# Optimization experiments

Measured on AMD Instinct MI355X. Metric: run time of the kernel, lower is better.

Reference implementation:

```python
import jax, jax.numpy as jnp
import numpy as np

N_NODES = 20000
N_EDGES = 640000
D = 64        # node / edge feature dim
H = 128       # MLP hidden dim


def setup_inputs() -> dict:
    key = jax.random.key(0)
    ks = jax.random.split(key, 12)
    inp = {
        "x": jax.random.normal(ks[0], (N_NODES, D), dtype=jnp.float32),
        "edge_index": jax.random.randint(ks[1], (2, N_EDGES), 0, N_NODES, dtype=jnp.int64),
        "edge_attr": jax.random.normal(ks[2], (N_EDGES, D), dtype=jnp.float32),
        "f": jax.random.normal(ks[3], (N_NODES, D), dtype=jnp.float32),
        # edge MLP: concat(x_src, x_dest, edge_attr) = 3D -> H -> D
        "We1": jax.random.normal(ks[4], (3 * D, H), dtype=jnp.float32) / np.sqrt(3 * D),
        "be1": jnp.zeros((H,), dtype=jnp.float32),
        "We2": jax.random.normal(ks[5], (H, D), dtype=jnp.float32) / np.sqrt(H),
        "be2": jnp.zeros((D,), dtype=jnp.float32),
        # node MLP: concat(x, agg, f) = 3D -> H -> D
        "Wn1": jax.random.normal(ks[6], (3 * D, H), dtype=jnp.float32) / np.sqrt(3 * D),
        "bn1": jnp.zeros((H,), dtype=jnp.float32),
        "Wn2": jax.random.normal(ks[7], (H, D), dtype=jnp.float32) / np.sqrt(H),
        "bn2": jnp.zeros((D,), dtype=jnp.float32),
    }
    return inp


def reference(x, edge_index, edge_attr, f, We1, be1, We2, be2, Wn1, bn1, Wn2, bn2):
    src, dest = edge_index[0], edge_index[1]
    # edge model: MLP over gathered src/dest node features + edge attrs
    e_in = jnp.concatenate([x[src], x[dest], edge_attr], axis=-1)      # [E, 3D]
    e_h = jax.nn.relu(e_in @ We1 + be1)                                 # [E, H]
    edge_out = e_h @ We2 + be2                                          # [E, D]
    # node model: scatter-add edge messages to dest, then MLP
    agg = jax.ops.segment_sum(edge_out, dest, num_segments=N_NODES)    # [N, D]
    n_in = jnp.concatenate([x, agg, f], axis=-1)                        # [N, 3D]
    n_h = jax.nn.relu(n_in @ Wn1 + bn1)                                 # [N, H]
    x_out = n_h @ Wn2 + bn2                                             # [N, D]
    return (x_out, edge_out)
```

## Files before the change

### kernel.cpp

```cpp
#include <hip/hip_runtime.h>

#define NE 640000
#define NN 20000
#define SEI 200
#define SEH 136
#define SEO 100

typedef __attribute__((ext_vector_type(8))) short s16x8;
typedef __attribute__((ext_vector_type(4))) short s16x4;
typedef __attribute__((ext_vector_type(4))) float f32x4;

typedef const __attribute__((ext_vector_type(4))) float cf32x4;

#define BARRIER_LGKM() do {                                   \
    asm volatile("s_waitcnt lgkmcnt(0)" ::: "memory");        \
    __builtin_amdgcn_s_barrier();                             \
    __builtin_amdgcn_sched_barrier(0);                        \
  } while (0)

__device__ __forceinline__ short f2bf(float f) {
  unsigned int u = __float_as_uint(f);
  u += 0x7fffu + ((u >> 16) & 1u);
  return (short)(u >> 16);
}

__device__ __forceinline__ s16x8 cvt8(f32x4 a, f32x4 b) {
  s16x8 o;
  o[0]=f2bf(a[0]); o[1]=f2bf(a[1]); o[2]=f2bf(a[2]); o[3]=f2bf(a[3]);
  o[4]=f2bf(b[0]); o[5]=f2bf(b[1]); o[6]=f2bf(b[2]); o[7]=f2bf(b[3]);
  return o;
}

__device__ __forceinline__ void load_wfrags_lds(const float* W1, const float* W2,
                                                const float* b1, const float* b2,
                                                short* smem, int t,
                                                int wv, int r, int g,
                                                s16x8 w1f[2][6], s16x8 w2f[4],
                                                f32x4 b1r[2], f32x4* b2r) {
  #pragma unroll
  for (int i = 0; i < 24; ++i) {
    int idx4 = t + i * 256;
    f32x4 v = ((cf32x4*)W1)[idx4];
    s16x4 pk; pk[0]=f2bf(v[0]); pk[1]=f2bf(v[1]); pk[2]=f2bf(v[2]); pk[3]=f2bf(v[3]);
    *(s16x4*)&smem[idx4 * 4] = pk;
  }
  __syncthreads();
  #pragma unroll
  for (int nn = 0; nn < 2; ++nn) {
    const int h = (wv*2+nn)*16 + r;
    #pragma unroll
    for (int kk = 0; kk < 6; ++kk) {
      s16x8 wf;
      #pragma unroll
      for (int i = 0; i < 8; ++i) wf[i] = smem[(kk*32 + g*8 + i)*128 + h];
      w1f[nn][kk] = wf;
    }
    b1r[nn] = *(cf32x4*)(b1 + (wv*2+nn)*16 + g*4);
  }
  __syncthreads();
  #pragma unroll
  for (int i = 0; i < 8; ++i) {
    int idx4 = t + i * 256;
    f32x4 v = ((cf32x4*)W2)[idx4];
    s16x4 pk; pk[0]=f2bf(v[0]); pk[1]=f2bf(v[1]); pk[2]=f2bf(v[2]); pk[3]=f2bf(v[3]);
    *(s16x4*)&smem[idx4 * 4] = pk;
  }
  __syncthreads();
  {
    const int h2 = wv*16 + r;
    #pragma unroll
    for (int kk = 0; kk < 4; ++kk) {
      s16x8 wf;
      #pragma unroll
      for (int i = 0; i < 8; ++i) wf[i] = smem[(kk*32 + g*8 + i)*64 + h2];
      w2f[kk] = wf;
    }
    *b2r = *(cf32x4*)(b2 + wv*16 + g*4);
  }
  __syncthreads();
}


__global__ void count_kernel(const int* __restrict__ eidx, int* __restrict__ cursor) {
  const int4* d4 = (const int4*)(eidx + NE);
  int i = blockIdx.x * blockDim.x + threadIdx.x;
  if (i < NE / 4) {
    int4 d = d4[i];
    atomicAdd(&cursor[d.x], 1);
    atomicAdd(&cursor[d.y], 1);
    atomicAdd(&cursor[d.z], 1);
    atomicAdd(&cursor[d.w], 1);
  }
}

__global__ __launch_bounds__(1024)
void scan_kernel(int* __restrict__ cursor, int* __restrict__ offs) {
  __shared__ int cnt[20480];
  __shared__ int part[1024];
  const int t = threadIdx.x;
  for (int i = t; i < 20480; i += 1024)
    cnt[i] = (i < NN) ? cursor[i] : 0;
  __syncthreads();
  const int lo = t * 20;
  int s = 0;
  #pragma unroll
  for (int k = 0; k < 20; ++k) s += cnt[lo + k];
  part[t] = s;
  __syncthreads();
  for (int d = 1; d < 1024; d <<= 1) {
    int u = (t >= d) ? part[t - d] : 0;
    __syncthreads();
    part[t] += u;
    __syncthreads();
  }
  int run = part[t] - s;
  #pragma unroll
  for (int k = 0; k < 20; ++k) {
    int c = cnt[lo + k];
    cnt[lo + k] = run;
    run += c;
  }
  __syncthreads();
  for (int i = t; i < NN; i += 1024) {
    int v = cnt[i];
    offs[i] = v;
    cursor[i] = v;
  }
  if (t == 1023) offs[NN] = NE;
}

__global__ void scatter_kernel(const int* __restrict__ eidx,
                               int* __restrict__ cursor, int* __restrict__ elist) {
  const int4* d4 = (const int4*)(eidx + NE);
  int i = blockIdx.x * blockDim.x + threadIdx.x;
  if (i < NE / 4) {
    int4 d = d4[i];
    const int e = i * 4;
    elist[atomicAdd(&cursor[d.x], 1)] = e;
    elist[atomicAdd(&cursor[d.y], 1)] = e + 1;
    elist[atomicAdd(&cursor[d.z], 1)] = e + 2;
    elist[atomicAdd(&cursor[d.w], 1)] = e + 3;
  }
}

#define LOAD_ROWS(sv, dv, ee) do {                                        \
    cf32x4* ps_ = (cf32x4*)(x  + (size_t)(sv)*64 + p*16);                 \
    cf32x4* pd_ = (cf32x4*)(x  + (size_t)(dv)*64 + p*16);                 \
    cf32x4* pe_ = (cf32x4*)(ea + (size_t)(ee)*64 + p*16);                 \
    L[0]=ps_[0]; L[1]=ps_[1]; L[2]=ps_[2];  L[3]=ps_[3];                  \
    L[4]=pd_[0]; L[5]=pd_[1]; L[6]=pd_[2];  L[7]=pd_[3];                  \
    L[8]=pe_[0]; L[9]=pe_[1]; L[10]=pe_[2]; L[11]=pe_[3];                 \
  } while (0)

#define WRITE_EIN(buf) do {                                               \
    short* stg_ = (buf) + el*SEI + p*16;                                  \
    ((s16x8*)stg_)[0]       = cvt8(L[0], L[1]);                           \
    ((s16x8*)stg_)[1]       = cvt8(L[2], L[3]);                           \
    ((s16x8*)(stg_+64))[0]  = cvt8(L[4], L[5]);                           \
    ((s16x8*)(stg_+64))[1]  = cvt8(L[6], L[7]);                           \
    ((s16x8*)(stg_+128))[0] = cvt8(L[8], L[9]);                           \
    ((s16x8*)(stg_+128))[1] = cvt8(L[10], L[11]);                         \
  } while (0)

__global__ __launch_bounds__(256, 2)
void edge_kernel(const float* __restrict__ x, const int* __restrict__ eidx,
                 const float* __restrict__ ea, const int* __restrict__ elist,
                 const float* __restrict__ We1, const float* __restrict__ be1,
                 const float* __restrict__ We2, const float* __restrict__ be2,
                 float* __restrict__ edge_out, float* __restrict__ agg)
{
  __shared__ __align__(16) char smem[69632];
  short* sEin0 = (short*)smem;
  short* sEin1 = (short*)(smem + 25600);
  short* sEh   = (short*)(smem + 51200);
  int* sDest0  = (int*)(smem + 68608);
  int* sDest1  = (int*)(smem + 68864);
  int* sEid0   = (int*)(smem + 69120);
  int* sEid1   = (int*)(smem + 69376);

  const int t = threadIdx.x;
  const int wv = t >> 6, lane = t & 63;
  const int r = lane & 15, g = lane >> 4;

  s16x8 w1f[2][6], w2f[4];
  f32x4 b1r[2], b2r;
  load_wfrags_lds(We1, We2, be1, be2, (short*)smem, t, wv, r, g,
                  w1f, w2f, b1r, &b2r);

  const int el = t >> 2, p = t & 3;
  const f32x4 zero = {0.f, 0.f, 0.f, 0.f};

  const int b = blockIdx.x;
  const int t0 = b * 19 + (b < 272 ? b : 272);
  const int t1 = t0 + (b < 272 ? 20 : 19);

  f32x4 L[12];
  int eW = 0, dW = 0;
  int eI = 0, sI = 0, dI = 0;
  int tile = t0;

  {
    int e0 = elist[(tile << 6) + el];
    int s0 = eidx[e0], d0 = eidx[NE + e0];
    LOAD_ROWS(s0, d0, e0);
    WRITE_EIN(sEin0);
    if (p == 0) { sDest0[el] = d0; sEid0[el] = e0; }
    if (tile + 1 < t1) {
      eW = elist[((tile + 1) << 6) + el];
      int sv = eidx[eW]; dW = eidx[NE + eW];
      LOAD_ROWS(sv, dW, eW);
    }
    if (tile + 2 < t1) {
      eI = elist[((tile + 2) << 6) + el];
      sI = eidx[eI]; dI = eidx[NE + eI];
    }
  }
  BARRIER_LGKM();

  int cur = 0;
  while (tile < t1) {
    const short* Ecur = cur ? sEin1 : sEin0;
    short* Enxt = cur ? sEin0 : sEin1;
    float* EoutC = (float*)(cur ? (smem + 25600) : smem);
    const int* sDestC = cur ? sDest1 : sDest0;
    const int* sEidC  = cur ? sEid1  : sEid0;
    int* sDestN = cur ? sDest0 : sDest1;
    int* sEidN  = cur ? sEid0  : sEid1;

    const int tW = tile + 1, tI = tile + 2, tX = tile + 3;
    if (tW < t1) {
      WRITE_EIN(Enxt);
      if (p == 0) { sDestN[el] = dW; sEidN[el] = eW; }
    }
    if (tI < t1) { LOAD_ROWS(sI, dI, eI); eW = eI; dW = dI; }
    if (tX < t1) {
      eI = elist[(tX << 6) + el];
      sI = eidx[eI]; dI = eidx[NE + eI];
    }

    f32x4 acc1[2][4];
    #pragma unroll
    for (int nn = 0; nn < 2; ++nn)
      #pragma unroll
      for (int j = 0; j < 4; ++j) acc1[nn][j] = zero;
    #pragma unroll
    for (int kk = 0; kk < 6; ++kk) {
      #pragma unroll
      for (int j = 0; j < 4; ++j) {
        s16x8 ef = *(const s16x8*)&Ecur[(j*16 + r)*SEI + kk*32 + g*8];
        acc1[0][j] = __builtin_amdgcn_mfma_f32_16x16x32_bf16(w1f[0][kk], ef, acc1[0][j], 0, 0, 0);
        acc1[1][j] = __builtin_amdgcn_mfma_f32_16x16x32_bf16(w1f[1][kk], ef, acc1[1][j], 0, 0, 0);
      }
    }
    #pragma unroll
    for (int nn = 0; nn < 2; ++nn)
      #pragma unroll
      for (int j = 0; j < 4; ++j) {
        s16x4 pk;
        #pragma unroll
        for (int q = 0; q < 4; ++q) {
          float v = acc1[nn][j][q] + b1r[nn][q];
          pk[q] = f2bf(v > 0.f ? v : 0.f);
        }
        *(s16x4*)&sEh[(j*16 + r)*SEH + (wv*2+nn)*16 + g*4] = pk;
      }
    BARRIER_LGKM();

    #pragma unroll
    for (int j = 0; j < 4; ++j) {
      f32x4 a2 = zero;
      #pragma unroll
      for (int kk = 0; kk < 4; ++kk) {
        s16x8 hf = *(const s16x8*)&sEh[(j*16 + r)*SEH + kk*32 + g*8];
        a2 = __builtin_amdgcn_mfma_f32_16x16x32_bf16(w2f[kk], hf, a2, 0, 0, 0);
      }
      a2 += b2r;
      const int eg = sEidC[j*16 + r];
      *(f32x4*)&edge_out[(size_t)eg*64 + wv*16 + g*4] = a2;
      *(f32x4*)&EoutC[(j*16 + r)*SEO + wv*16 + g*4] = a2;
    }
    BARRIER_LGKM();

    {
      const int row0 = wv * 16;
      float acc = EoutC[row0*SEO + lane];
      int dcur = sDestC[row0];
      #pragma unroll
      for (int k = 1; k < 16; ++k) {
        const int dn = sDestC[row0 + k];
        const float v = EoutC[(row0 + k)*SEO + lane];
        if (dn != dcur) {
          unsafeAtomicAdd(&agg[(size_t)dcur*64 + lane], acc);
          acc = v; dcur = dn;
        } else {
          acc += v;
        }
      }
      unsafeAtomicAdd(&agg[(size_t)dcur*64 + lane], acc);
    }
    cur ^= 1;
    tile = tW;
  }
}

__global__ __launch_bounds__(256, 2)
void node_kernel(const float* __restrict__ x, const float* agg,
                 const float* __restrict__ f,
                 const float* __restrict__ Wn1, const float* __restrict__ bn1,
                 const float* __restrict__ Wn2, const float* __restrict__ bn2,
                 float* x_out)
{
  __shared__ __align__(16) char smem[49152];
  short* sEin = (short*)smem;
  short* sEh  = (short*)(smem + 25600);

  const int t = threadIdx.x;
  const int wv = t >> 6, lane = t & 63;
  const int r = lane & 15, g = lane >> 4;

  s16x8 w1f[2][6], w2f[4];
  f32x4 b1r[2], b2r;
  load_wfrags_lds(Wn1, Wn2, bn1, bn2, (short*)smem, t, wv, r, g,
                  w1f, w2f, b1r, &b2r);

  const int el = t >> 2, p = t & 3;
  const f32x4 zero = {0.f, 0.f, 0.f, 0.f};
  const int nT = (NN + 63) / 64;

  for (int tile = blockIdx.x; tile < nT; tile += (int)gridDim.x) {
    const int base = tile << 6;
    const int i = base + el;

    f32x4 L[12];
    if (i < NN) {
      cf32x4* ps_ = (cf32x4*)(x   + (size_t)i*64 + p*16);
      cf32x4* pa_ = (cf32x4*)(agg + (size_t)i*64 + p*16);
      cf32x4* pf_ = (cf32x4*)(f   + (size_t)i*64 + p*16);
      L[0]=ps_[0]; L[1]=ps_[1]; L[2]=ps_[2];  L[3]=ps_[3];
      L[4]=pa_[0]; L[5]=pa_[1]; L[6]=pa_[2];  L[7]=pa_[3];
      L[8]=pf_[0]; L[9]=pf_[1]; L[10]=pf_[2]; L[11]=pf_[3];
    } else {
      #pragma unroll
      for (int q = 0; q < 12; ++q) L[q] = zero;
    }
    WRITE_EIN(sEin);
    __syncthreads();

    f32x4 acc1[2][4];
    #pragma unroll
    for (int nn = 0; nn < 2; ++nn)
      #pragma unroll
      for (int j = 0; j < 4; ++j) acc1[nn][j] = zero;
    #pragma unroll
    for (int kk = 0; kk < 6; ++kk) {
      #pragma unroll
      for (int j = 0; j < 4; ++j) {
        s16x8 ef = *(const s16x8*)&sEin[(j*16 + r)*SEI + kk*32 + g*8];
        acc1[0][j] = __builtin_amdgcn_mfma_f32_16x16x32_bf16(w1f[0][kk], ef, acc1[0][j], 0, 0, 0);
        acc1[1][j] = __builtin_amdgcn_mfma_f32_16x16x32_bf16(w1f[1][kk], ef, acc1[1][j], 0, 0, 0);
      }
    }
    #pragma unroll
    for (int nn = 0; nn < 2; ++nn)
      #pragma unroll
      for (int j = 0; j < 4; ++j) {
        s16x4 pk;
        #pragma unroll
        for (int q = 0; q < 4; ++q) {
          float v = acc1[nn][j][q] + b1r[nn][q];
          pk[q] = f2bf(v > 0.f ? v : 0.f);
        }
        *(s16x4*)&sEh[(j*16 + r)*SEH + (wv*2+nn)*16 + g*4] = pk;
      }
    __syncthreads();

    #pragma unroll
    for (int j = 0; j < 4; ++j) {
      f32x4 a2 = zero;
      #pragma unroll
      for (int kk = 0; kk < 4; ++kk) {
        s16x8 hf = *(const s16x8*)&sEh[(j*16 + r)*SEH + kk*32 + g*8];
        a2 = __builtin_amdgcn_mfma_f32_16x16x32_bf16(w2f[kk], hf, a2, 0, 0, 0);
      }
      const int row = base + j*16 + r;
      if (row < NN) {
        f32x4 v = a2 + b2r;
        *(f32x4*)&x_out[(size_t)row*64 + wv*16 + g*4] = v;
      }
    }
  }
}

extern "C" void kernel_launch(void* const* d_in, const int* in_sizes, int n_in,
                              void* d_out, int out_size, void* d_ws, size_t ws_size,
                              hipStream_t stream) {
  const float* x   = (const float*)d_in[0];
  const int*   ei  = (const int*)d_in[1];
  const float* ea  = (const float*)d_in[2];
  const float* f   = (const float*)d_in[3];
  const float* We1 = (const float*)d_in[4];
  const float* be1 = (const float*)d_in[5];
  const float* We2 = (const float*)d_in[6];
  const float* be2 = (const float*)d_in[7];
  const float* Wn1 = (const float*)d_in[8];
  const float* bn1 = (const float*)d_in[9];
  const float* Wn2 = (const float*)d_in[10];
  const float* bn2 = (const float*)d_in[11];

  float* x_out    = (float*)d_out;
  float* edge_out = x_out + (size_t)NN * 64;

  int* cursor = (int*)d_ws;
  int* offs   = cursor + NN;
  int* elist  = offs + NN + 8;

  hipMemsetAsync(x_out, 0, (size_t)NN * 64 * sizeof(float), stream);
  hipMemsetAsync(cursor, 0, NN * sizeof(int), stream);
  count_kernel<<<625, 256, 0, stream>>>(ei, cursor);
  scan_kernel<<<1, 1024, 0, stream>>>(cursor, offs);
  scatter_kernel<<<625, 256, 0, stream>>>(ei, cursor, elist);
  edge_kernel<<<512, 256, 0, stream>>>(x, ei, ea, elist, We1, be1, We2, be2,
                                       edge_out, x_out);
  node_kernel<<<105, 256, 0, stream>>>(x, x_out, f, Wn1, bn1, Wn2, bn2, x_out);
}
```

Baseline: 227.4 us.

## Widen edge kernel to 512 threads, splitting MLP work across eight waves

The edge kernel moves from 256 to 512 threads per block. Each of the eight waves now owns one 16-column slice of the hidden layer and half of the output-row tiles, and each thread gathers half as many row bytes. This cuts per-thread registers (weight fragments, accumulators, load buffers) so more waves can hide the latency of the irregular gathers. The cost is more barrier participants per block and smaller per-wave segment reductions, which issue more atomics to agg.

```diff
diff --git a/kernel.cpp b/kernel.cpp
--- a/kernel.cpp
+++ b/kernel.cpp
@@ -35,8 +35,56 @@
                                                 const float* b1, const float* b2,
                                                 short* smem, int t,
                                                 int wv, int r, int g,
-                                                s16x8 w1f[2][6], s16x8 w2f[4],
-                                                f32x4 b1r[2], f32x4* b2r) {
+                                                s16x8 w1f[6], s16x8 w2f[4],
+                                                f32x4* b1r, f32x4* b2r) {
+  #pragma unroll
+  for (int i = 0; i < 12; ++i) {
+    int idx4 = t + i * 512;
+    f32x4 v = ((cf32x4*)W1)[idx4];
+    s16x4 pk; pk[0]=f2bf(v[0]); pk[1]=f2bf(v[1]); pk[2]=f2bf(v[2]); pk[3]=f2bf(v[3]);
+    *(s16x4*)&smem[idx4 * 4] = pk;
+  }
+  __syncthreads();
+  {
+    const int h = wv*16 + r;
+    #pragma unroll
+    for (int kk = 0; kk < 6; ++kk) {
+      s16x8 wf;
+      #pragma unroll
+      for (int i = 0; i < 8; ++i) wf[i] = smem[(kk*32 + g*8 + i)*128 + h];
+      w1f[kk] = wf;
+    }
+    *b1r = *(cf32x4*)(b1 + wv*16 + g*4);
+  }
+  __syncthreads();
+  #pragma unroll
+  for (int i = 0; i < 4; ++i) {
+    int idx4 = t + i * 512;
+    f32x4 v = ((cf32x4*)W2)[idx4];
+    s16x4 pk; pk[0]=f2bf(v[0]); pk[1]=f2bf(v[1]); pk[2]=f2bf(v[2]); pk[3]=f2bf(v[3]);
+    *(s16x4*)&smem[idx4 * 4] = pk;
+  }
+  __syncthreads();
+  {
+    const int h2 = (wv >> 1)*16 + r;
+    #pragma unroll
+    for (int kk = 0; kk < 4; ++kk) {
+      s16x8 wf;
+      #pragma unroll
+      for (int i = 0; i < 8; ++i) wf[i] = smem[(kk*32 + g*8 + i)*64 + h2];
+      w2f[kk] = wf;
+    }
+    *b2r = *(cf32x4*)(b2 + (wv >> 1)*16 + g*4);
+  }
+  __syncthreads();
+}
+
+__device__ __forceinline__ void load_wfrags_lds4(const float* W1, const float* W2,
+                                                 const float* b1, const float* b2,
+                                                 short* smem, int t,
+                                                 int wv, int r, int g,
+                                                 s16x8 w1f[2][6], s16x8 w2f[4],
+                                                 f32x4 b1r[2], f32x4* b2r) {
   #pragma unroll
   for (int i = 0; i < 24; ++i) {
     int idx4 = t + i * 256;
@@ -144,25 +192,22 @@
 }
 
 #define LOAD_ROWS(sv, dv, ee) do {                                        \
-    cf32x4* ps_ = (cf32x4*)(x  + (size_t)(sv)*64 + p*16);                 \
-    cf32x4* pd_ = (cf32x4*)(x  + (size_t)(dv)*64 + p*16);                 \
-    cf32x4* pe_ = (cf32x4*)(ea + (size_t)(ee)*64 + p*16);                 \
-    L[0]=ps_[0]; L[1]=ps_[1]; L[2]=ps_[2];  L[3]=ps_[3];                  \
-    L[4]=pd_[0]; L[5]=pd_[1]; L[6]=pd_[2];  L[7]=pd_[3];                  \
-    L[8]=pe_[0]; L[9]=pe_[1]; L[10]=pe_[2]; L[11]=pe_[3];                 \
+    cf32x4* ps_ = (cf32x4*)(x  + (size_t)(sv)*64 + p*8);                  \
+    cf32x4* pd_ = (cf32x4*)(x  + (size_t)(dv)*64 + p*8);                  \
+    cf32x4* pe_ = (cf32x4*)(ea + (size_t)(ee)*64 + p*8);                  \
+    L[0]=ps_[0]; L[1]=ps_[1];                                             \
+    L[2]=pd_[0]; L[3]=pd_[1];                                             \
+    L[4]=pe_[0]; L[5]=pe_[1];                                             \
   } while (0)
 
 #define WRITE_EIN(buf) do {                                               \
-    short* stg_ = (buf) + el*SEI + p*16;                                  \
-    ((s16x8*)stg_)[0]       = cvt8(L[0], L[1]);                           \
-    ((s16x8*)stg_)[1]       = cvt8(L[2], L[3]);                           \
-    ((s16x8*)(stg_+64))[0]  = cvt8(L[4], L[5]);                           \
-    ((s16x8*)(stg_+64))[1]  = cvt8(L[6], L[7]);                           \
-    ((s16x8*)(stg_+128))[0] = cvt8(L[8], L[9]);                           \
-    ((s16x8*)(stg_+128))[1] = cvt8(L[10], L[11]);                         \
+    short* stg_ = (buf) + el*SEI + p*8;                                   \
+    *(s16x8*)stg_         = cvt8(L[0], L[1]);                             \
+    *(s16x8*)(stg_ + 64)  = cvt8(L[2], L[3]);                             \
+    *(s16x8*)(stg_ + 128) = cvt8(L[4], L[5]);                             \
   } while (0)
 
-__global__ __launch_bounds__(256, 2)
+__global__ __launch_bounds__(512, 2)
 void edge_kernel(const float* __restrict__ x, const int* __restrict__ eidx,
                  const float* __restrict__ ea, const int* __restrict__ elist,
                  const float* __restrict__ We1, const float* __restrict__ be1,
@@ -182,19 +227,19 @@
   const int wv = t >> 6, lane = t & 63;
   const int r = lane & 15, g = lane >> 4;
 
-  s16x8 w1f[2][6], w2f[4];
-  f32x4 b1r[2], b2r;
+  s16x8 w1f[6], w2f[4];
+  f32x4 b1r, b2r;
   load_wfrags_lds(We1, We2, be1, be2, (short*)smem, t, wv, r, g,
-                  w1f, w2f, b1r, &b2r);
-
-  const int el = t >> 2, p = t & 3;
+                  w1f, w2f, &b1r, &b2r);
+
+  const int el = t >> 3, p = t & 7;
   const f32x4 zero = {0.f, 0.f, 0.f, 0.f};
 
   const int b = blockIdx.x;
   const int t0 = b * 19 + (b < 272 ? b : 272);
   const int t1 = t0 + (b < 272 ? 20 : 19);
 
-  f32x4 L[12];
+  f32x4 L[6];
   int eW = 0, dW = 0;
   int eI = 0, sI = 0, dI = 0;
   int tile = t0;
@@ -238,55 +283,54 @@
       sI = eidx[eI]; dI = eidx[NE + eI];
     }
 
-    f32x4 acc1[2][4];
-    #pragma unroll
-    for (int nn = 0; nn < 2; ++nn)
-      #pragma unroll
-      for (int j = 0; j < 4; ++j) acc1[nn][j] = zero;
+    f32x4 acc1[4];
+    #pragma unroll
+    for (int j = 0; j < 4; ++j) acc1[j] = zero;
     #pragma unroll
     for (int kk = 0; kk < 6; ++kk) {
       #pragma unroll
       for (int j = 0; j < 4; ++j) {
         s16x8 ef = *(const s16x8*)&Ecur[(j*16 + r)*SEI + kk*32 + g*8];
-        acc1[0][j] = __builtin_amdgcn_mfma_f32_16x16x32_bf16(w1f[0][kk], ef, acc1[0][j], 0, 0, 0);
-        acc1[1][j] = __builtin_amdgcn_mfma_f32_16x16x32_bf16(w1f[1][kk], ef, acc1[1][j], 0, 0, 0);
-      }
-    }
-    #pragma unroll
-    for (int nn = 0; nn < 2; ++nn)
-      #pragma unroll
-      for (int j = 0; j < 4; ++j) {
-        s16x4 pk;
+        acc1[j] = __builtin_amdgcn_mfma_f32_16x16x32_bf16(w1f[kk], ef, acc1[j], 0, 0, 0);
+      }
+    }
+    #pragma unroll
+    for (int j = 0; j < 4; ++j) {
+      s16x4 pk;
+      #pragma unroll
+      for (int q = 0; q < 4; ++q) {
+        float v = acc1[j][q] + b1r[q];
+        pk[q] = f2bf(v > 0.f ? v : 0.f);
+      }
+      *(s16x4*)&sEh[(j*16 + r)*SEH + wv*16 + g*4] = pk;
+    }
+    BARRIER_LGKM();
+
+    {
+      const int dt = wv >> 1;
+      #pragma unroll
+      for (int jj = 0; jj < 2; ++jj) {
+        const int row = ((wv & 1)*2 + jj)*16 + r;
+        f32x4 a2 = zero;
         #pragma unroll
-        for (int q = 0; q < 4; ++q) {
-          float v = acc1[nn][j][q] + b1r[nn][q];
-          pk[q] = f2bf(v > 0.f ? v : 0.f);
+        for (int kk = 0; kk < 4; ++kk) {
+          s16x8 hf = *(const s16x8*)&sEh[row*SEH + kk*32 + g*8];
+          a2 = __builtin_amdgcn_mfma_f32_16x16x32_bf16(w2f[kk], hf, a2, 0, 0, 0);
         }
-        *(s16x4*)&sEh[(j*16 + r)*SEH + (wv*2+nn)*16 + g*4] = pk;
-      }
+        a2 += b2r;
+        const int eg = sEidC[row];
+        *(f32x4*)&edge_out[(size_t)eg*64 + dt*16 + g*4] = a2;
+        *(f32x4*)&EoutC[row*SEO + dt*16 + g*4] = a2;
+      }
+    }
     BARRIER_LGKM();
 
-    #pragma unroll
-    for (int j = 0; j < 4; ++j) {
-      f32x4 a2 = zero;
-      #pragma unroll
-      for (int kk = 0; kk < 4; ++kk) {
-        s16x8 hf = *(const s16x8*)&sEh[(j*16 + r)*SEH + kk*32 + g*8];
-        a2 = __builtin_amdgcn_mfma_f32_16x16x32_bf16(w2f[kk], hf, a2, 0, 0, 0);
-      }
-      a2 += b2r;
-      const int eg = sEidC[j*16 + r];
-      *(f32x4*)&edge_out[(size_t)eg*64 + wv*16 + g*4] = a2;
-      *(f32x4*)&EoutC[(j*16 + r)*SEO + wv*16 + g*4] = a2;
-    }
-    BARRIER_LGKM();
-
     {
-      const int row0 = wv * 16;
+      const int row0 = wv * 8;
       float acc = EoutC[row0*SEO + lane];
       int dcur = sDestC[row0];
       #pragma unroll
-      for (int k = 1; k < 16; ++k) {
+      for (int k = 1; k < 8; ++k) {
         const int dn = sDestC[row0 + k];
         const float v = EoutC[(row0 + k)*SEO + lane];
         if (dn != dcur) {
@@ -320,8 +364,8 @@
 
   s16x8 w1f[2][6], w2f[4];
   f32x4 b1r[2], b2r;
-  load_wfrags_lds(Wn1, Wn2, bn1, bn2, (short*)smem, t, wv, r, g,
-                  w1f, w2f, b1r, &b2r);
+  load_wfrags_lds4(Wn1, Wn2, bn1, bn2, (short*)smem, t, wv, r, g,
+                   w1f, w2f, b1r, &b2r);
 
   const int el = t >> 2, p = t & 3;
   const f32x4 zero = {0.f, 0.f, 0.f, 0.f};
@@ -343,7 +387,15 @@
       #pragma unroll
       for (int q = 0; q < 12; ++q) L[q] = zero;
     }
-    WRITE_EIN(sEin);
+    {
+      short* stg_ = sEin + el*SEI + p*16;
+      ((s16x8*)stg_)[0]       = cvt8(L[0], L[1]);
+      ((s16x8*)stg_)[1]       = cvt8(L[2], L[3]);
+      ((s16x8*)(stg_+64))[0]  = cvt8(L[4], L[5]);
+      ((s16x8*)(stg_+64))[1]  = cvt8(L[6], L[7]);
+      ((s16x8*)(stg_+128))[0] = cvt8(L[8], L[9]);
+      ((s16x8*)(stg_+128))[1] = cvt8(L[10], L[11]);
+    }
     __syncthreads();
 
     f32x4 acc1[2][4];
@@ -419,7 +471,7 @@
   count_kernel<<<625, 256, 0, stream>>>(ei, cursor);
   scan_kernel<<<1, 1024, 0, stream>>>(cursor, offs);
   scatter_kernel<<<625, 256, 0, stream>>>(ei, cursor, elist);
-  edge_kernel<<<512, 256, 0, stream>>>(x, ei, ea, elist, We1, be1, We2, be2,
+  edge_kernel<<<512, 512, 0, stream>>>(x, ei, ea, elist, We1, be1, We2, be2,
                                        edge_out, x_out);
   node_kernel<<<105, 256, 0, stream>>>(x, x_out, f, Wn1, bn1, Wn2, bn2, x_out);
 }
```

Measured after the change: 257.6 us. 1.13x slower.

## Single-buffer edge tile in LDS, shuffle-based segmented reduction, launch more blocks

Applied to the files above, without the earlier changes.

Cuts edge_kernel shared memory from about 68KB to 48KB by keeping one edge-input tile buffer instead of two. The write of the next tile is moved to after the first GEMM barrier, so it overlaps the second GEMM. The LDS staging of edge outputs for scatter-add is replaced by a 16-lane shuffle segmented scan on registers, with atomics issued from segment tails. The grid grows from 512 to 768 blocks so three blocks fit per CU, trading per-block prefetch overlap and adding more per-element atomics (4 scalar atomics per lane) for higher occupancy.

```diff
diff --git a/kernel.cpp b/kernel.cpp
--- a/kernel.cpp
+++ b/kernel.cpp
@@ -4,7 +4,6 @@
 #define NN 20000
 #define SEI 200
 #define SEH 136
-#define SEO 100
 
 typedef __attribute__((ext_vector_type(8))) short s16x8;
 typedef __attribute__((ext_vector_type(4))) short s16x4;
@@ -169,14 +168,13 @@
                  const float* __restrict__ We2, const float* __restrict__ be2,
                  float* __restrict__ edge_out, float* __restrict__ agg)
 {
-  __shared__ __align__(16) char smem[69632];
-  short* sEin0 = (short*)smem;
-  short* sEin1 = (short*)(smem + 25600);
-  short* sEh   = (short*)(smem + 51200);
-  int* sDest0  = (int*)(smem + 68608);
-  int* sDest1  = (int*)(smem + 68864);
-  int* sEid0   = (int*)(smem + 69120);
-  int* sEid1   = (int*)(smem + 69376);
+  __shared__ __align__(16) char smem[49152];
+  short* sEin  = (short*)smem;
+  short* sEh   = (short*)(smem + 25600);
+  int* sDest0  = (int*)(smem + 43008);
+  int* sDest1  = (int*)(smem + 43264);
+  int* sEid0   = (int*)(smem + 43520);
+  int* sEid1   = (int*)(smem + 43776);
 
   const int t = threadIdx.x;
   const int wv = t >> 6, lane = t & 63;
@@ -191,8 +189,8 @@
   const f32x4 zero = {0.f, 0.f, 0.f, 0.f};
 
   const int b = blockIdx.x;
-  const int t0 = b * 19 + (b < 272 ? b : 272);
-  const int t1 = t0 + (b < 272 ? 20 : 19);
+  const int t0 = b * 13 + (b < 16 ? b : 16);
+  const int t1 = t0 + (b < 16 ? 14 : 13);
 
   f32x4 L[12];
   int eW = 0, dW = 0;
@@ -203,7 +201,7 @@
     int e0 = elist[(tile << 6) + el];
     int s0 = eidx[e0], d0 = eidx[NE + e0];
     LOAD_ROWS(s0, d0, e0);
-    WRITE_EIN(sEin0);
+    WRITE_EIN(sEin);
     if (p == 0) { sDest0[el] = d0; sEid0[el] = e0; }
     if (tile + 1 < t1) {
       eW = elist[((tile + 1) << 6) + el];
@@ -219,24 +217,11 @@
 
   int cur = 0;
   while (tile < t1) {
-    const short* Ecur = cur ? sEin1 : sEin0;
-    short* Enxt = cur ? sEin0 : sEin1;
-    float* EoutC = (float*)(cur ? (smem + 25600) : smem);
     const int* sDestC = cur ? sDest1 : sDest0;
     const int* sEidC  = cur ? sEid1  : sEid0;
     int* sDestN = cur ? sDest0 : sDest1;
     int* sEidN  = cur ? sEid0  : sEid1;
-
     const int tW = tile + 1, tI = tile + 2, tX = tile + 3;
-    if (tW < t1) {
-      WRITE_EIN(Enxt);
-      if (p == 0) { sDestN[el] = dW; sEidN[el] = eW; }
-    }
-    if (tI < t1) { LOAD_ROWS(sI, dI, eI); eW = eI; dW = dI; }
-    if (tX < t1) {
-      eI = elist[(tX << 6) + el];
-      sI = eidx[eI]; dI = eidx[NE + eI];
-    }
 
     f32x4 acc1[2][4];
     #pragma unroll
@@ -247,7 +232,7 @@
     for (int kk = 0; kk < 6; ++kk) {
       #pragma unroll
       for (int j = 0; j < 4; ++j) {
-        s16x8 ef = *(const s16x8*)&Ecur[(j*16 + r)*SEI + kk*32 + g*8];
+        s16x8 ef = *(const s16x8*)&sEin[(j*16 + r)*SEI + kk*32 + g*8];
         acc1[0][j] = __builtin_amdgcn_mfma_f32_16x16x32_bf16(w1f[0][kk], ef, acc1[0][j], 0, 0, 0);
         acc1[1][j] = __builtin_amdgcn_mfma_f32_16x16x32_bf16(w1f[1][kk], ef, acc1[1][j], 0, 0, 0);
       }
@@ -266,6 +251,16 @@
       }
     BARRIER_LGKM();
 
+    if (tW < t1) {
+      WRITE_EIN(sEin);
+      if (p == 0) { sDestN[el] = dW; sEidN[el] = eW; }
+    }
+    if (tI < t1) { LOAD_ROWS(sI, dI, eI); eW = eI; dW = dI; }
+    if (tX < t1) {
+      eI = elist[(tX << 6) + el];
+      sI = eidx[eI]; dI = eidx[NE + eI];
+    }
+
     #pragma unroll
     for (int j = 0; j < 4; ++j) {
       f32x4 a2 = zero;
@@ -277,27 +272,25 @@
       a2 += b2r;
       const int eg = sEidC[j*16 + r];
       *(f32x4*)&edge_out[(size_t)eg*64 + wv*16 + g*4] = a2;
-      *(f32x4*)&EoutC[(j*16 + r)*SEO + wv*16 + g*4] = a2;
+
+      int d = sDestC[j*16 + r];
+      f32x4 v = a2;
+      #pragma unroll
+      for (int off = 1; off < 16; off <<= 1) {
+        int du = __shfl_up(d, off, 16);
+        f32x4 u;
+        #pragma unroll
+        for (int q = 0; q < 4; ++q) u[q] = __shfl_up(v[q], off, 16);
+        if (r >= off && du == d) v += u;
+      }
+      const bool tail = (r == 15) || (sDestC[j*16 + r + 1] != d);
+      if (tail) {
+        #pragma unroll
+        for (int q = 0; q < 4; ++q)
+          unsafeAtomicAdd(&agg[(size_t)d*64 + wv*16 + g*4 + q], v[q]);
+      }
     }
     BARRIER_LGKM();
-
-    {
-      const int row0 = wv * 16;
-      float acc = EoutC[row0*SEO + lane];
-      int dcur = sDestC[row0];
-      #pragma unroll
-      for (int k = 1; k < 16; ++k) {
-        const int dn = sDestC[row0 + k];
-        const float v = EoutC[(row0 + k)*SEO + lane];
-        if (dn != dcur) {
-          unsafeAtomicAdd(&agg[(size_t)dcur*64 + lane], acc);
-          acc = v; dcur = dn;
-        } else {
-          acc += v;
-        }
-      }
-      unsafeAtomicAdd(&agg[(size_t)dcur*64 + lane], acc);
-    }
     cur ^= 1;
     tile = tW;
   }
@@ -419,7 +412,7 @@
   count_kernel<<<625, 256, 0, stream>>>(ei, cursor);
   scan_kernel<<<1, 1024, 0, stream>>>(cursor, offs);
   scatter_kernel<<<625, 256, 0, stream>>>(ei, cursor, elist);
-  edge_kernel<<<512, 256, 0, stream>>>(x, ei, ea, elist, We1, be1, We2, be2,
+  edge_kernel<<<768, 256, 0, stream>>>(x, ei, ea, elist, We1, be1, We2, be2,
                                        edge_out, x_out);
   node_kernel<<<105, 256, 0, stream>>>(x, x_out, f, Wn1, bn1, Wn2, bn2, x_out);
 }
```

Result: slower. 274.6 us (+20.8%).
